# Optimization experiments

Measured on AMD Instinct MI355X. Metric: run time of the kernel, lower is better.

The kernel has to match this reference:

```python
import jax, jax.numpy as jnp
import numpy as np

EPS = 1e-12  # torch F.normalize eps


def setup_inputs() -> dict:
    key = jax.random.key(0)
    k1, k2 = jax.random.split(key)
    B, C, H, W = 8, 512, 96, 144
    M, D = 512, 512
    query_source = jax.random.normal(k1, (B, C, H, W), dtype=jnp.float32)
    mem = jax.random.uniform(k2, (M, D), dtype=jnp.float32)
    # Memory params are initialized as F.normalize(rand, dim=1)
    mem = mem / jnp.maximum(jnp.linalg.norm(mem, axis=1, keepdims=True), EPS)
    return {"query_source": query_source, "memory": mem}


def reference(query_source, memory):
    # forward(query_source, keys, only_update=False, query_target=None, fusion_keys=None)
    # -> self.read(normalize(query_source).permute(0,2,3,1), memory['3_0'])
    # L2-normalize over channel dim (dim=1), like F.normalize
    norm = jnp.linalg.norm(query_source, axis=1, keepdims=True)
    q = query_source / jnp.maximum(norm, EPS)
    q = jnp.transpose(q, (0, 2, 3, 1))  # [B, H, W, D]
    B, H, W, D = q.shape
    M = memory.shape[0]
    # get_score: score = query @ mem^T, then softmax over tokens (dim 0) and slots (dim 1)
    score = jnp.einsum('nd,md->nm', q.reshape(B * H * W, D), memory)  # [N, M]
    softmax_score_query = jax.nn.softmax(score, axis=0)
    softmax_score_memory = jax.nn.softmax(score, axis=1)
    # read: updated_query = score_memory.detach() @ memory
    updated_query = jax.lax.stop_gradient(softmax_score_memory) @ memory  # [N, D]
    updated_query = updated_query.reshape(B, H, W, D).transpose(0, 3, 1, 2)  # [B, D, H, W]
    return updated_query, softmax_score_query, softmax_score_memory
```

## Files before the change

kernel.cpp:

```cpp
#include <hip/hip_runtime.h>
#include <hip/hip_bf16.h>
#include <cstdint>
#include <cstddef>

#define HWIMG 13824
#define NTOK  110592
#define CDIM  512

typedef float  floatx4  __attribute__((ext_vector_type(4)));
typedef __bf16 bf16x8   __attribute__((ext_vector_type(8)));
typedef unsigned short ushortx8 __attribute__((ext_vector_type(8)));

__device__ __forceinline__ unsigned short f2bf(float f) {
  unsigned int u = __float_as_uint(f);
  u += 0x7FFFu + ((u >> 16) & 1u);
  return (unsigned short)(u >> 16);
}

#define GLL16(g, l)                                                                \
  __builtin_amdgcn_global_load_lds((const __attribute__((address_space(1))) void*)(g), \
                                   (__attribute__((address_space(3))) void*)(l), 16, 0, 0)

__global__ __launch_bounds__(256) void convert_mem_kernel(
    const float* __restrict__ mem, unsigned short* __restrict__ membf,
    unsigned short* __restrict__ memTbf) {
  int g = blockIdx.x * 256 + threadIdx.x;
  int m = g >> 9, d = g & 511;
  unsigned short b = f2bf(mem[g]);
  membf[g] = b;
  memTbf[d * 512 + m] = b;
}

__global__ __launch_bounds__(256) void normalize_kernel(
    const float* __restrict__ qs, unsigned short* __restrict__ qbf) {
  __shared__ float red[4][64];
  __shared__ float inv[64];
  __shared__ float tile[64][65];
  const int t = threadIdx.x;
  const int n0 = blockIdx.x * 64;
  const int b = n0 / HWIMG;
  const int r0 = n0 % HWIMG;
  const float* base = qs + (size_t)b * 512 * HWIMG + r0;
  const int tok = t & 63, cp = t >> 6;

  float ssq = 0.f;
  for (int c = cp; c < 512; c += 4) {
    float x = base[(size_t)c * HWIMG + tok];
    ssq += x * x;
  }
  red[cp][tok] = ssq;
  __syncthreads();
  if (t < 64) {
    float s = red[0][t] + red[1][t] + red[2][t] + red[3][t];
    inv[t] = 1.0f / fmaxf(sqrtf(s), 1e-12f);
  }
  __syncthreads();

  for (int cc = 0; cc < 8; cc++) {
#pragma unroll
    for (int i = 0; i < 16; i++) {
      int cl = (t >> 6) + i * 4;
      tile[cl][tok] = base[(size_t)(cc * 64 + cl) * HWIMG + tok];
    }
    __syncthreads();
    const int c_out = t & 63;
    const int tg = t >> 6;
#pragma unroll
    for (int i = 0; i < 16; i++) {
      int tk = tg * 16 + i;
      float v = tile[c_out][tk] * inv[tk];
      qbf[(size_t)(n0 + tk) * 512 + cc * 64 + c_out] = f2bf(v);
    }
    __syncthreads();
  }
}

#define GEMM_PROLOGUE(Aptr, Bptr)                                               \
  __shared__ unsigned short Alds[128 * 32];                                     \
  __shared__ unsigned short Blds[128 * 32];                                     \
  const int t = threadIdx.x;                                                    \
  const int lane = t & 63;                                                      \
  const int wid = t >> 6;                                                       \
  const int n0 = blockIdx.x * 128;                                              \
  const int m0 = blockIdx.y * 128;                                              \
  floatx4 acc[4][4];                                                            \
  {                                                                             \
    floatx4 z = {0.f, 0.f, 0.f, 0.f};                                           \
    for (int i = 0; i < 4; i++)                                                 \
      for (int j = 0; j < 4; j++) acc[i][j] = z;                                \
  }                                                                             \
  const int cid0 = t, cid1 = t + 256;                                           \
  const int row0 = ((cid0 >> 6) << 4) | (cid0 & 15);                            \
  const int row1 = ((cid1 >> 6) << 4) | (cid1 & 15);                            \
  const int qb0 = ((cid0 >> 4) & 3) << 4;                                       \
  const int qb1 = ((cid1 >> 4) & 3) << 4;                                       \
  const char* gA0 = (const char*)(Aptr) + (size_t)(n0 + row0) * 1024 + qb0;     \
  const char* gA1 = (const char*)(Aptr) + (size_t)(n0 + row1) * 1024 + qb1;     \
  const char* gB0 = (const char*)(Bptr) + (size_t)(m0 + row0) * 1024 + qb0;     \
  const char* gB1 = (const char*)(Bptr) + (size_t)(m0 + row1) * 1024 + qb1;     \
  char* lA0 = (char*)Alds + cid0 * 16;                                          \
  char* lA1 = (char*)Alds + cid1 * 16;                                          \
  char* lB0 = (char*)Blds + cid0 * 16;                                          \
  char* lB1 = (char*)Blds + cid1 * 16;                                          \
  const int am = (wid & 1) * 4;                                                 \
  const int bn = (wid >> 1) * 4;                                                \
  for (int kb = 0; kb < 1024; kb += 64) {     \
    GLL16(gA0 + kb, lA0);                                                       \
    GLL16(gA1 + kb, lA1);                                                       \
    GLL16(gB0 + kb, lB0);                                                       \
    GLL16(gB1 + kb, lB1);                                                       \
    asm volatile("s_waitcnt vmcnt(0)" ::: "memory");                            \
    __syncthreads();                                                            \
    bf16x8 af[4], bfv[4];                                                       \
    for (int i = 0; i < 4; i++)                                                 \
      af[i] = *(const bf16x8*)&Alds[((am + i) * 64 + lane) * 8];                \
    for (int j = 0; j < 4; j++)                                                 \
      bfv[j] = *(const bf16x8*)&Blds[((bn + j) * 64 + lane) * 8];               \
    for (int i = 0; i < 4; i++)                                                 \
      for (int j = 0; j < 4; j++)                                               \
        acc[i][j] =                                                             \
            __builtin_amdgcn_mfma_f32_16x16x32_bf16(af[i], bfv[j], acc[i][j], 0, 0, 0); \
    __syncthreads();                                                            \
  }

__global__ __launch_bounds__(256, 2) void gemm1_kernel(
    const unsigned short* __restrict__ A, const unsigned short* __restrict__ Bm,
    float* __restrict__ E, float* __restrict__ colsum, float* __restrict__ rowsum) {
  __shared__ float cs_lds[128];
  __shared__ float rs_lds[128];
  if (threadIdx.x < 128) { cs_lds[threadIdx.x] = 0.f; rs_lds[threadIdx.x] = 0.f; }
  GEMM_PROLOGUE(A, Bm)
  const int quad = lane >> 4, li = lane & 15;
  const int wm = (wid & 1) * 64, wn = (wid >> 1) * 64;
  float cp[4] = {0.f, 0.f, 0.f, 0.f};
#pragma unroll
  for (int i = 0; i < 4; i++) {
#pragma unroll
    for (int r = 0; r < 4; r++) {
      float rowacc = 0.f;
      const int row = n0 + wm + i * 16 + quad * 4 + r;
#pragma unroll
      for (int j = 0; j < 4; j++) {
        float e = __expf(acc[i][j][r]);
        const int col = m0 + wn + j * 16 + li;
        E[(size_t)row * 512 + col] = e;
        cp[j] += e;
        rowacc += e;
      }
      rowacc += __shfl_xor(rowacc, 1, 64);
      rowacc += __shfl_xor(rowacc, 2, 64);
      rowacc += __shfl_xor(rowacc, 4, 64);
      rowacc += __shfl_xor(rowacc, 8, 64);
      if (li == 0) atomicAdd(&rs_lds[wm + i * 16 + quad * 4 + r], rowacc);
    }
  }
#pragma unroll
  for (int j = 0; j < 4; j++) {
    float c = cp[j];
    c += __shfl_xor(c, 16, 64);
    c += __shfl_xor(c, 32, 64);
    if (lane < 16) atomicAdd(&cs_lds[wn + j * 16 + li], c);
  }
  __syncthreads();
  if (t < 128) {
    atomicAdd(&rowsum[n0 + t], rs_lds[t]);
    atomicAdd(&colsum[m0 + t], cs_lds[t]);
  }
}

__global__ __launch_bounds__(256, 2) void gemm2_kernel(
    const unsigned short* __restrict__ P, const unsigned short* __restrict__ BmT,
    float* __restrict__ out0) {
  GEMM_PROLOGUE(P, BmT)
  const int quad = lane >> 4, li = lane & 15;
  const int wm = (wid & 1) * 64, wn = (wid >> 1) * 64;
  const int bimg = n0 / HWIMG;
  const int r0 = n0 % HWIMG;
#pragma unroll
  for (int i = 0; i < 4; i++) {
    const int rb = r0 + wm + i * 16 + quad * 4;
#pragma unroll
    for (int j = 0; j < 4; j++) {
      const int col = m0 + wn + j * 16 + li;
      *(floatx4*)&out0[(size_t)(bimg * 512 + col) * HWIMG + rb] = acc[i][j];
    }
  }
}

__global__ __launch_bounds__(256) void finalize_kernel(
    float* __restrict__ E, const float* __restrict__ colsum,
    const float* __restrict__ rowsum, float* __restrict__ out2,
    unsigned short* __restrict__ pbf) {
  const int t = threadIdx.x;
  const int lane = t & 63, wid = t >> 6;
  const int wg = blockIdx.x * 4 + wid;
  const int c0 = lane * 8;
  floatx4 one = {1.f, 1.f, 1.f, 1.f};
  floatx4 rc0 = one / *(const floatx4*)&colsum[c0];
  floatx4 rc1 = one / *(const floatx4*)&colsum[c0 + 4];
  for (int it = 0; it < 64; it++) {
    const int row = wg * 64 + it;
    const size_t off = (size_t)row * 512 + c0;
    floatx4 e0 = *(const floatx4*)&E[off];
    floatx4 e1 = *(const floatx4*)&E[off + 4];
    float rr = 1.0f / rowsum[row];
    floatx4 o2a = e0 * rr, o2b = e1 * rr;
    *(floatx4*)&E[off]     = e0 * rc0;
    *(floatx4*)&E[off + 4] = e1 * rc1;
    *(floatx4*)&out2[off]     = o2a;
    *(floatx4*)&out2[off + 4] = o2b;
    ushortx8 p;
    p[0] = f2bf(o2a[0]); p[1] = f2bf(o2a[1]); p[2] = f2bf(o2a[2]); p[3] = f2bf(o2a[3]);
    p[4] = f2bf(o2b[0]); p[5] = f2bf(o2b[1]); p[6] = f2bf(o2b[2]); p[7] = f2bf(o2b[3]);
    *(ushortx8*)&pbf[off] = p;
  }
}

extern "C" void kernel_launch(void* const* d_in, const int* in_sizes, int n_in,
                              void* d_out, int out_size, void* d_ws, size_t ws_size,
                              hipStream_t stream) {
  const float* qs  = (const float*)d_in[0];
  const float* mem = (const float*)d_in[1];

  float* out0 = (float*)d_out;
  float* out1 = out0 + (size_t)NTOK * 512;
  float* out2 = out1 + (size_t)NTOK * 512;

  char* ws = (char*)d_ws;
  unsigned short* qbf    = (unsigned short*)ws;
  unsigned short* pbf    = qbf;
  unsigned short* membf  = (unsigned short*)(ws + 113246208);
  unsigned short* memTbf = (unsigned short*)(ws + 113770496);
  float* colsum          = (float*)(ws + 114294784);
  float* rowsum          = (float*)(ws + 114296832);

  hipMemsetAsync(colsum, 0, 2048 + 442368, stream);
  convert_mem_kernel<<<1024, 256, 0, stream>>>(mem, membf, memTbf);
  normalize_kernel<<<NTOK / 64, 256, 0, stream>>>(qs, qbf);
  gemm1_kernel<<<dim3(NTOK / 128, 4), 256, 0, stream>>>(qbf, membf, out1, colsum, rowsum);
  finalize_kernel<<<NTOK / 256, 256, 0, stream>>>(out1, colsum, rowsum, out2, pbf);
  gemm2_kernel<<<dim3(NTOK / 128, 4), 256, 0, stream>>>(pbf, memTbf, out0);
}
```

Baseline: 1.263 ms.

## Store exp scores as bf16, fold row normalization into gemm2 epilogue

gemm1 now writes the exponentiated scores as a bf16 scratch buffer instead of fp32 into out1. Each block loops over all four memory tiles, so row sums stay in registers and are written without global atomics. Finalize reads the bf16 scores and writes out1 and out2 once, no longer re-reading and rewriting fp32 E or producing a separate P buffer. gemm2 consumes the unnormalized bf16 exponentials and scales by 1/rowsum in its epilogue, and the K loop now stages 128-wide chunks to halve barriers. The cost is that out1 and out2 are computed from bf16-rounded exponentials, which loses precision, and each block occupies more LDS.

```diff
diff --git a/kernel.cpp b/kernel.cpp
--- a/kernel.cpp
+++ b/kernel.cpp
@@ -15,6 +15,9 @@
   unsigned int u = __float_as_uint(f);
   u += 0x7FFFu + ((u >> 16) & 1u);
   return (unsigned short)(u >> 16);
+}
+__device__ __forceinline__ float bf2f(unsigned short u) {
+  return __uint_as_float(((unsigned int)u) << 16);
 }
 
 #define GLL16(g, l)                                                                \
@@ -75,144 +78,194 @@
   }
 }
 
-#define GEMM_PROLOGUE(Aptr, Bptr)                                               \
-  __shared__ unsigned short Alds[128 * 32];                                     \
-  __shared__ unsigned short Blds[128 * 32];                                     \
-  const int t = threadIdx.x;                                                    \
-  const int lane = t & 63;                                                      \
-  const int wid = t >> 6;                                                       \
-  const int n0 = blockIdx.x * 128;                                              \
-  const int m0 = blockIdx.y * 128;                                              \
-  floatx4 acc[4][4];                                                            \
-  {                                                                             \
-    floatx4 z = {0.f, 0.f, 0.f, 0.f};                                           \
-    for (int i = 0; i < 4; i++)                                                 \
-      for (int j = 0; j < 4; j++) acc[i][j] = z;                                \
-  }                                                                             \
-  const int cid0 = t, cid1 = t + 256;                                           \
-  const int row0 = ((cid0 >> 6) << 4) | (cid0 & 15);                            \
-  const int row1 = ((cid1 >> 6) << 4) | (cid1 & 15);                            \
-  const int qb0 = ((cid0 >> 4) & 3) << 4;                                       \
-  const int qb1 = ((cid1 >> 4) & 3) << 4;                                       \
-  const char* gA0 = (const char*)(Aptr) + (size_t)(n0 + row0) * 1024 + qb0;     \
-  const char* gA1 = (const char*)(Aptr) + (size_t)(n0 + row1) * 1024 + qb1;     \
-  const char* gB0 = (const char*)(Bptr) + (size_t)(m0 + row0) * 1024 + qb0;     \
-  const char* gB1 = (const char*)(Bptr) + (size_t)(m0 + row1) * 1024 + qb1;     \
-  char* lA0 = (char*)Alds + cid0 * 16;                                          \
-  char* lA1 = (char*)Alds + cid1 * 16;                                          \
-  char* lB0 = (char*)Blds + cid0 * 16;                                          \
-  char* lB1 = (char*)Blds + cid1 * 16;                                          \
-  const int am = (wid & 1) * 4;                                                 \
-  const int bn = (wid >> 1) * 4;                                                \
-  for (int kb = 0; kb < 1024; kb += 64) {     \
-    GLL16(gA0 + kb, lA0);                                                       \
-    GLL16(gA1 + kb, lA1);                                                       \
-    GLL16(gB0 + kb, lB0);                                                       \
-    GLL16(gB1 + kb, lB1);                                                       \
-    asm volatile("s_waitcnt vmcnt(0)" ::: "memory");                            \
-    __syncthreads();                                                            \
-    bf16x8 af[4], bfv[4];                                                       \
-    for (int i = 0; i < 4; i++)                                                 \
-      af[i] = *(const bf16x8*)&Alds[((am + i) * 64 + lane) * 8];                \
-    for (int j = 0; j < 4; j++)                                                 \
-      bfv[j] = *(const bf16x8*)&Blds[((bn + j) * 64 + lane) * 8];               \
-    for (int i = 0; i < 4; i++)                                                 \
-      for (int j = 0; j < 4; j++)                                               \
-        acc[i][j] =                                                             \
-            __builtin_amdgcn_mfma_f32_16x16x32_bf16(af[i], bfv[j], acc[i][j], 0, 0, 0); \
-    __syncthreads();                                                            \
-  }
-
-__global__ __launch_bounds__(256, 2) void gemm1_kernel(
+#define GEMM_STAGE8(gAp, gBp, kb)                                          \
+  GLL16((gAp) + (kb), lA);                                                 \
+  GLL16((gAp) + (kb) + 32768, lA + 4096);                                  \
+  GLL16((gAp) + (kb) + 65536, lA + 8192);                                  \
+  GLL16((gAp) + (kb) + 98304, lA + 12288);                                 \
+  GLL16((gBp) + (kb), lB);                                                 \
+  GLL16((gBp) + (kb) + 32768, lB + 4096);                                  \
+  GLL16((gBp) + (kb) + 65536, lB + 8192);                                  \
+  GLL16((gBp) + (kb) + 98304, lB + 12288);
+
+#define GEMM_K_LOOP(gAp, gBp)                                              \
+  for (int kb = 0; kb < 1024; kb += 128) {                                 \
+    GEMM_STAGE8(gAp, gBp, kb)                                              \
+    asm volatile("s_waitcnt vmcnt(0)" ::: "memory");                       \
+    __syncthreads();                                                       \
+    _Pragma("unroll")                                                      \
+    for (int h = 0; h < 2; h++) {                                          \
+      bf16x8 af[4], bfv[4];                                                \
+      _Pragma("unroll")                                                    \
+      for (int i = 0; i < 4; i++)                                          \
+        af[i] = *(const bf16x8*)&Alds[((((am + i) * 2 + h) << 6) | lane) * 8]; \
+      _Pragma("unroll")                                                    \
+      for (int j = 0; j < 4; j++)                                          \
+        bfv[j] = *(const bf16x8*)&Blds[((((bn + j) * 2 + h) << 6) | lane) * 8]; \
+      _Pragma("unroll")                                                    \
+      for (int i = 0; i < 4; i++)                                          \
+        _Pragma("unroll")                                                  \
+        for (int j = 0; j < 4; j++)                                        \
+          acc[i][j] = __builtin_amdgcn_mfma_f32_16x16x32_bf16(             \
+              af[i], bfv[j], acc[i][j], 0, 0, 0);                          \
+    }                                                                      \
+    __syncthreads();                                                       \
+  }
+
+#define GEMM_COMMON_DECLS                                                  \
+  __shared__ unsigned short Alds[128 * 64];                                \
+  __shared__ unsigned short Blds[128 * 64];                                \
+  const int t = threadIdx.x;                                               \
+  const int lane = t & 63, wid = t >> 6;                                   \
+  const int quad = lane >> 4, li = lane & 15;                              \
+  const int n0 = blockIdx.x * 128;                                         \
+  const int am = (wid & 1) * 4, bn = (wid >> 1) * 4;                       \
+  const int wm = (wid & 1) * 64, wn = (wid >> 1) * 64;                     \
+  const int row0 = ((t >> 7) << 4) | (t & 15);                             \
+  const int koff = ((t >> 6) & 1) * 64 + ((t >> 4) & 3) * 16;              \
+  char* lA = (char*)Alds + t * 16;                                         \
+  char* lB = (char*)Blds + t * 16;
+
+__global__ __launch_bounds__(256) void gemm1_kernel(
     const unsigned short* __restrict__ A, const unsigned short* __restrict__ Bm,
-    float* __restrict__ E, float* __restrict__ colsum, float* __restrict__ rowsum) {
-  __shared__ float cs_lds[128];
+    unsigned short* __restrict__ Ebf, float* __restrict__ colsum,
+    float* __restrict__ rowsum) {
+  __shared__ float cs_lds[512];
   __shared__ float rs_lds[128];
-  if (threadIdx.x < 128) { cs_lds[threadIdx.x] = 0.f; rs_lds[threadIdx.x] = 0.f; }
-  GEMM_PROLOGUE(A, Bm)
-  const int quad = lane >> 4, li = lane & 15;
-  const int wm = (wid & 1) * 64, wn = (wid >> 1) * 64;
-  float cp[4] = {0.f, 0.f, 0.f, 0.f};
+  GEMM_COMMON_DECLS
+  cs_lds[t] = 0.f; cs_lds[t + 256] = 0.f;
+  if (t < 128) rs_lds[t] = 0.f;
+  const char* gA = (const char*)A + (size_t)(n0 + row0) * 1024 + koff;
+  const char* gB0 = (const char*)Bm + (size_t)row0 * 1024 + koff;
+  float racc[4][4];
+#pragma unroll
+  for (int i = 0; i < 4; i++)
+#pragma unroll
+    for (int r = 0; r < 4; r++) racc[i][r] = 0.f;
+
+#pragma unroll 1
+  for (int mt = 0; mt < 4; mt++) {
+    floatx4 acc[4][4];
+    {
+      floatx4 z = {0.f, 0.f, 0.f, 0.f};
+#pragma unroll
+      for (int i = 0; i < 4; i++)
+#pragma unroll
+        for (int j = 0; j < 4; j++) acc[i][j] = z;
+    }
+    const char* gB = gB0 + (size_t)mt * 131072;
+    GEMM_K_LOOP(gA, gB)
+
+    float cp[4] = {0.f, 0.f, 0.f, 0.f};
+#pragma unroll
+    for (int i = 0; i < 4; i++) {
+#pragma unroll
+      for (int r = 0; r < 4; r++) {
+        const int row = n0 + wm + i * 16 + quad * 4 + r;
+        float rowacc = 0.f;
+#pragma unroll
+        for (int j = 0; j < 4; j++) {
+          float e = __expf(acc[i][j][r]);
+          const int col = mt * 128 + wn + j * 16 + li;
+          Ebf[(size_t)row * 512 + col] = f2bf(e);
+          cp[j] += e;
+          rowacc += e;
+        }
+        racc[i][r] += rowacc;
+      }
+    }
+#pragma unroll
+    for (int j = 0; j < 4; j++) {
+      float c = cp[j];
+      c += __shfl_xor(c, 16, 64);
+      c += __shfl_xor(c, 32, 64);
+      if (lane < 16) atomicAdd(&cs_lds[mt * 128 + wn + j * 16 + li], c);
+    }
+  }
+
 #pragma unroll
   for (int i = 0; i < 4; i++) {
 #pragma unroll
     for (int r = 0; r < 4; r++) {
-      float rowacc = 0.f;
-      const int row = n0 + wm + i * 16 + quad * 4 + r;
-#pragma unroll
-      for (int j = 0; j < 4; j++) {
-        float e = __expf(acc[i][j][r]);
-        const int col = m0 + wn + j * 16 + li;
-        E[(size_t)row * 512 + col] = e;
-        cp[j] += e;
-        rowacc += e;
-      }
-      rowacc += __shfl_xor(rowacc, 1, 64);
-      rowacc += __shfl_xor(rowacc, 2, 64);
-      rowacc += __shfl_xor(rowacc, 4, 64);
-      rowacc += __shfl_xor(rowacc, 8, 64);
-      if (li == 0) atomicAdd(&rs_lds[wm + i * 16 + quad * 4 + r], rowacc);
-    }
-  }
-#pragma unroll
-  for (int j = 0; j < 4; j++) {
-    float c = cp[j];
-    c += __shfl_xor(c, 16, 64);
-    c += __shfl_xor(c, 32, 64);
-    if (lane < 16) atomicAdd(&cs_lds[wn + j * 16 + li], c);
+      float v = racc[i][r];
+      v += __shfl_xor(v, 1, 64);
+      v += __shfl_xor(v, 2, 64);
+      v += __shfl_xor(v, 4, 64);
+      v += __shfl_xor(v, 8, 64);
+      if (li == 0) atomicAdd(&rs_lds[wm + i * 16 + quad * 4 + r], v);
+    }
   }
   __syncthreads();
-  if (t < 128) {
-    atomicAdd(&rowsum[n0 + t], rs_lds[t]);
-    atomicAdd(&colsum[m0 + t], cs_lds[t]);
-  }
-}
-
-__global__ __launch_bounds__(256, 2) void gemm2_kernel(
+  if (t < 128) rowsum[n0 + t] = rs_lds[t];
+  atomicAdd(&colsum[t], cs_lds[t]);
+  atomicAdd(&colsum[t + 256], cs_lds[t + 256]);
+}
+
+__global__ __launch_bounds__(256) void gemm2_kernel(
     const unsigned short* __restrict__ P, const unsigned short* __restrict__ BmT,
-    float* __restrict__ out0) {
-  GEMM_PROLOGUE(P, BmT)
-  const int quad = lane >> 4, li = lane & 15;
-  const int wm = (wid & 1) * 64, wn = (wid >> 1) * 64;
+    const float* __restrict__ rowsum, float* __restrict__ out0) {
+  GEMM_COMMON_DECLS
+  const char* gA = (const char*)P + (size_t)(n0 + row0) * 1024 + koff;
+  const char* gB0 = (const char*)BmT + (size_t)row0 * 1024 + koff;
+  floatx4 rinv[4];
+#pragma unroll
+  for (int i = 0; i < 4; i++) {
+    floatx4 one = {1.f, 1.f, 1.f, 1.f};
+    rinv[i] = one / *(const floatx4*)&rowsum[n0 + wm + i * 16 + quad * 4];
+  }
   const int bimg = n0 / HWIMG;
   const int r0 = n0 % HWIMG;
-#pragma unroll
-  for (int i = 0; i < 4; i++) {
-    const int rb = r0 + wm + i * 16 + quad * 4;
-#pragma unroll
-    for (int j = 0; j < 4; j++) {
-      const int col = m0 + wn + j * 16 + li;
-      *(floatx4*)&out0[(size_t)(bimg * 512 + col) * HWIMG + rb] = acc[i][j];
+
+#pragma unroll 1
+  for (int mt = 0; mt < 4; mt++) {
+    floatx4 acc[4][4];
+    {
+      floatx4 z = {0.f, 0.f, 0.f, 0.f};
+#pragma unroll
+      for (int i = 0; i < 4; i++)
+#pragma unroll
+        for (int j = 0; j < 4; j++) acc[i][j] = z;
+    }
+    const char* gB = gB0 + (size_t)mt * 131072;
+    GEMM_K_LOOP(gA, gB)
+
+#pragma unroll
+    for (int i = 0; i < 4; i++) {
+      const int rb = r0 + wm + i * 16 + quad * 4;
+#pragma unroll
+      for (int j = 0; j < 4; j++) {
+        const int col = mt * 128 + wn + j * 16 + li;
+        *(floatx4*)&out0[(size_t)(bimg * 512 + col) * HWIMG + rb] =
+            acc[i][j] * rinv[i];
+      }
     }
   }
 }
 
 __global__ __launch_bounds__(256) void finalize_kernel(
-    float* __restrict__ E, const float* __restrict__ colsum,
-    const float* __restrict__ rowsum, float* __restrict__ out2,
-    unsigned short* __restrict__ pbf) {
+    const unsigned short* __restrict__ Ebf, const float* __restrict__ colsum,
+    const float* __restrict__ rowsum, float* __restrict__ out1,
+    float* __restrict__ out2) {
   const int t = threadIdx.x;
   const int lane = t & 63, wid = t >> 6;
-  const int wg = blockIdx.x * 4 + wid;
+  const int rowbase = (blockIdx.x * 4 + wid) * 16;
   const int c0 = lane * 8;
   floatx4 one = {1.f, 1.f, 1.f, 1.f};
   floatx4 rc0 = one / *(const floatx4*)&colsum[c0];
   floatx4 rc1 = one / *(const floatx4*)&colsum[c0 + 4];
-  for (int it = 0; it < 64; it++) {
-    const int row = wg * 64 + it;
+#pragma unroll 4
+  for (int it = 0; it < 16; it++) {
+    const int row = rowbase + it;
     const size_t off = (size_t)row * 512 + c0;
-    floatx4 e0 = *(const floatx4*)&E[off];
-    floatx4 e1 = *(const floatx4*)&E[off + 4];
+    ushortx8 ev = *(const ushortx8*)&Ebf[off];
+    floatx4 e0, e1;
+    e0[0] = bf2f(ev[0]); e0[1] = bf2f(ev[1]); e0[2] = bf2f(ev[2]); e0[3] = bf2f(ev[3]);
+    e1[0] = bf2f(ev[4]); e1[1] = bf2f(ev[5]); e1[2] = bf2f(ev[6]); e1[3] = bf2f(ev[7]);
     float rr = 1.0f / rowsum[row];
-    floatx4 o2a = e0 * rr, o2b = e1 * rr;
-    *(floatx4*)&E[off]     = e0 * rc0;
-    *(floatx4*)&E[off + 4] = e1 * rc1;
-    *(floatx4*)&out2[off]     = o2a;
-    *(floatx4*)&out2[off + 4] = o2b;
-    ushortx8 p;
-    p[0] = f2bf(o2a[0]); p[1] = f2bf(o2a[1]); p[2] = f2bf(o2a[2]); p[3] = f2bf(o2a[3]);
-    p[4] = f2bf(o2b[0]); p[5] = f2bf(o2b[1]); p[6] = f2bf(o2b[2]); p[7] = f2bf(o2b[3]);
-    *(ushortx8*)&pbf[off] = p;
+    *(floatx4*)&out1[off]     = e0 * rc0;
+    *(floatx4*)&out1[off + 4] = e1 * rc1;
+    *(floatx4*)&out2[off]     = e0 * rr;
+    *(floatx4*)&out2[off + 4] = e1 * rr;
   }
 }
 
@@ -228,16 +281,16 @@
 
   char* ws = (char*)d_ws;
   unsigned short* qbf    = (unsigned short*)ws;
-  unsigned short* pbf    = qbf;
-  unsigned short* membf  = (unsigned short*)(ws + 113246208);
-  unsigned short* memTbf = (unsigned short*)(ws + 113770496);
-  float* colsum          = (float*)(ws + 114294784);
-  float* rowsum          = (float*)(ws + 114296832);
-
-  hipMemsetAsync(colsum, 0, 2048 + 442368, stream);
+  unsigned short* Ebf    = (unsigned short*)(ws + 113246208);
+  unsigned short* membf  = (unsigned short*)(ws + 226492416);
+  unsigned short* memTbf = (unsigned short*)(ws + 227016704);
+  float* colsum          = (float*)(ws + 227540992);
+  float* rowsum          = (float*)(ws + 227543040);
+
+  hipMemsetAsync(colsum, 0, 2048, stream);
   convert_mem_kernel<<<1024, 256, 0, stream>>>(mem, membf, memTbf);
   normalize_kernel<<<NTOK / 64, 256, 0, stream>>>(qs, qbf);
-  gemm1_kernel<<<dim3(NTOK / 128, 4), 256, 0, stream>>>(qbf, membf, out1, colsum, rowsum);
-  finalize_kernel<<<NTOK / 256, 256, 0, stream>>>(out1, colsum, rowsum, out2, pbf);
-  gemm2_kernel<<<dim3(NTOK / 128, 4), 256, 0, stream>>>(pbf, memTbf, out0);
-}
+  gemm1_kernel<<<NTOK / 128, 256, 0, stream>>>(qbf, membf, Ebf, colsum, rowsum);
+  finalize_kernel<<<NTOK / 64, 256, 0, stream>>>(Ebf, colsum, rowsum, out1, out2);
+  gemm2_kernel<<<NTOK / 128, 256, 0, stream>>>(Ebf, memTbf, rowsum, out0);
+}
```

New measurement: 1.229 ms. -2.7%, faster.
